# Kernel tuning notes

Hardware: AMD Instinct MI355X
Metric: run time of the kernel (lower is better)

## Reference

```python
import jax, jax.numpy as jnp
import numpy as np

B, N, D, H = 2048, 200, 128, 8

def setup_inputs() -> dict:
    key = jax.random.key(0)
    k1, k2, k3, k4, k5, k6 = jax.random.split(key, 6)
    return {
        "item_embedding": jax.random.normal(k1, (B, N, D), dtype=jnp.float32),
        "query_embedding": jax.random.normal(k2, (B, D), dtype=jnp.float32),
        "mask": jax.random.randint(k3, (B, N, 1), 0, 2).astype(bool),
        "Wq": jax.random.normal(k4, (D * H, D), dtype=jnp.float32) * 0.05,
        "bq": jax.random.normal(k5, (D * H,), dtype=jnp.float32) * 0.05,
        "Wr": jax.random.normal(k6, (1, H), dtype=jnp.float32) * 0.5,
    }

def reference(item_embedding, query_embedding, mask, Wq, bq, Wr):
    b = query_embedding.shape[0]
    # query projection + tanh, reshape to (B, D, H)
    pq = jnp.tanh(query_embedding @ Wq.T + bq).reshape(b, D, H)
    # batched dot: (B,N,D) @ (B,D,H) -> (B,N,H)
    dotted = jnp.einsum('bnd,bdh->bnh', item_embedding, pq)
    # head reduce: (B,N,H) @ (H,1) -> (B,N,1)
    reduced = dotted @ Wr.T
    scores = reduced - jnp.max(reduced, axis=1, keepdims=True)
    att = jnp.exp(scores) * mask
    denom = jnp.sum(att, axis=1, keepdims=True)
    weight = att / jnp.where(denom < 1e-7, denom + 1.0, denom)
    # weighted sum pooling -> (B, D)
    return jnp.sum(weight * item_embedding, axis=1)
```

## Files before the change

### kernel.cpp

```cpp
#include <hip/hip_runtime.h>

#define BB 2048
#define NN 200
#define DD 128
#define HH 8

__global__ __launch_bounds__(256) void proj_kernel(
    const float* __restrict__ q,
    const float* __restrict__ Wq,
    const float* __restrict__ bq,
    const float* __restrict__ Wr,
    float* __restrict__ v)
{
    __shared__ float wq_s[32][257];
    const int t  = threadIdx.x;
    const int jc = blockIdx.x;
    const int b0 = blockIdx.y * 16;
    const int j  = jc * 256 + t;

    float acc[16];
#pragma unroll
    for (int i = 0; i < 16; ++i) acc[i] = 0.f;

    for (int kt = 0; kt < 4; ++kt) {
        __syncthreads();
#pragma unroll
        for (int i = 0; i < 8; ++i) {
            int idx = t + 256 * i;
            int jj  = idx >> 3;
            int kf  = idx & 7;
            const float4 w4 = *(const float4*)(Wq + (size_t)(jc*256 + jj)*128 + kt*32 + kf*4);
            wq_s[kf*4+0][jj] = w4.x;
            wq_s[kf*4+1][jj] = w4.y;
            wq_s[kf*4+2][jj] = w4.z;
            wq_s[kf*4+3][jj] = w4.w;
        }
        __syncthreads();

        float wreg[32];
#pragma unroll
        for (int k = 0; k < 32; ++k) wreg[k] = wq_s[k][t];

#pragma unroll
        for (int bb = 0; bb < 16; ++bb) {
            const float* qrow = q + (size_t)(b0 + bb)*128 + kt*32;
            float s = 0.f;
#pragma unroll
            for (int k = 0; k < 32; ++k) s = fmaf(qrow[k], wreg[k], s);
            acc[bb] += s;
        }
    }

    const float bqj = bq[j];
    const float wrh = Wr[j & 7];
    const int   d   = j >> 3;
#pragma unroll
    for (int bb = 0; bb < 16; ++bb) {
        float p = tanhf(acc[bb] + bqj) * wrh;
        p += __shfl_xor(p, 1);
        p += __shfl_xor(p, 2);
        p += __shfl_xor(p, 4);
        if ((t & 7) == 0) v[(size_t)(b0 + bb)*128 + d] = p;
    }
}

__global__ __launch_bounds__(512) void attn_kernel(
    const float* __restrict__ item,
    const int*   __restrict__ mask,
    const float* __restrict__ v,
    float* __restrict__ out)
{
    __shared__ float item_s[64][132];
    __shared__ float red_s[64];
    __shared__ float w_s[64];
    __shared__ float o_s[4][128];

    const int t   = threadIdx.x;
    const int b   = blockIdx.x;
    const int seg = t & 31;
    const int l64 = t & 63;
    const int d   = t & 127;
    const int p   = t >> 7;

    const float4 vreg  = *(const float4*)(v + (size_t)b*128 + seg*4);
    const float* itemb = item + (size_t)b * (NN * 128);

    float m = -3e38f, lsum = 0.f, o_part = 0.f;

    for (int n0 = 0; n0 < NN; n0 += 64) {
        const int rows = min(64, NN - n0);
        __syncthreads();

#pragma unroll
        for (int i = 0; i < 4; ++i) {
            const int row = (t >> 5) + 16 * i;
            float4 f4 = make_float4(0.f, 0.f, 0.f, 0.f);
            if (row < rows)
                f4 = *(const float4*)(itemb + (size_t)(n0 + row)*128 + seg*4);
            float pp = f4.x*vreg.x + f4.y*vreg.y + f4.z*vreg.z + f4.w*vreg.w;
#pragma unroll
            for (int off = 16; off >= 1; off >>= 1)
                pp += __shfl_xor(pp, off);
            if (row < rows) {
                *(float4*)(&item_s[row][seg*4]) = f4;
                if (seg == 0) red_s[row] = pp;
            }
        }
        __syncthreads();

        float mv = (l64 < rows) ? red_s[l64] : -3e38f;
#pragma unroll
        for (int off = 32; off >= 1; off >>= 1)
            mv = fmaxf(mv, __shfl_xor(mv, off));
        const float new_m = fmaxf(m, mv);
        const float alpha = __expf(m - new_m);
        m = new_m;

        if (t < 64) {
            float w = 0.f;
            if (t < rows) {
                const int mk = mask[(size_t)b * NN + n0 + t];
                w = mk ? __expf(red_s[t] - new_m) : 0.f;
            }
            w_s[t] = w;
        }
        __syncthreads();

        float sv = w_s[l64];
#pragma unroll
        for (int off = 32; off >= 1; off >>= 1)
            sv += __shfl_xor(sv, off);
        lsum = lsum * alpha + sv;

        float acc = 0.f;
#pragma unroll
        for (int nn = 0; nn < 16; ++nn)
            acc = fmaf(w_s[p*16 + nn], item_s[p*16 + nn][d], acc);
        o_part = o_part * alpha + acc;
    }

    o_s[p][d] = o_part;
    __syncthreads();
    if (t < 128) {
        const float tot   = o_s[0][t] + o_s[1][t] + o_s[2][t] + o_s[3][t];
        const float denom = (lsum < 1e-7f) ? (lsum + 1.f) : lsum;
        out[(size_t)b * 128 + t] = tot / denom;
    }
}

extern "C" void kernel_launch(void* const* d_in, const int* in_sizes, int n_in,
                              void* d_out, int out_size, void* d_ws, size_t ws_size,
                              hipStream_t stream) {
    const float* item = (const float*)d_in[0];
    const float* q    = (const float*)d_in[1];
    const int*   mask = (const int*)  d_in[2];
    const float* Wq   = (const float*)d_in[3];
    const float* bq   = (const float*)d_in[4];
    const float* Wr   = (const float*)d_in[5];
    float* out = (float*)d_out;
    float* v   = (float*)d_ws;

    proj_kernel<<<dim3(4, 128), 256, 0, stream>>>(q, Wq, bq, Wr, v);
    attn_kernel<<<dim3(BB), 512, 0, stream>>>(item, mask, v, out);
}
```

Baseline: 345.2 us.

## Register-prefetch next item chunk and restructure attention into three chunks

```diff
diff --git a/kernel.cpp b/kernel.cpp
--- a/kernel.cpp
+++ b/kernel.cpp
@@ -4,6 +4,8 @@
 #define NN 200
 #define DD 128
 #define HH 8
+
+typedef float f4v __attribute__((ext_vector_type(4)));
 
 __global__ __launch_bounds__(256) void proj_kernel(
     const float* __restrict__ q,
@@ -64,51 +66,74 @@
     }
 }
 
-__global__ __launch_bounds__(512) void attn_kernel(
+__global__ __launch_bounds__(512, 8) void attn_kernel(
     const float* __restrict__ item,
     const int*   __restrict__ mask,
     const float* __restrict__ v,
     float* __restrict__ out)
 {
-    __shared__ float item_s[64][132];
-    __shared__ float red_s[64];
-    __shared__ float w_s[64];
-    __shared__ float o_s[4][128];
+    __shared__ float item_s[72][132];
+    __shared__ float red_s[72];
+    __shared__ float w_s[72];
 
-    const int t   = threadIdx.x;
-    const int b   = blockIdx.x;
-    const int seg = t & 31;
-    const int l64 = t & 63;
-    const int d   = t & 127;
-    const int p   = t >> 7;
+    const int t    = threadIdx.x;
+    const int b    = blockIdx.x;
+    const int seg  = t & 31;
+    const int half = t >> 5;
+    const int l64  = t & 63;
+    const int d    = t & 127;
+    const int p    = t >> 7;
 
-    const float4 vreg  = *(const float4*)(v + (size_t)b*128 + seg*4);
+    const f4v vreg = *(const f4v*)(v + (size_t)b*128 + seg*4);
     const float* itemb = item + (size_t)b * (NN * 128);
 
     float m = -3e38f, lsum = 0.f, o_part = 0.f;
 
-    for (int n0 = 0; n0 < NN; n0 += 64) {
-        const int rows = min(64, NN - n0);
+    f4v pre[5];
+#pragma unroll
+    for (int i = 0; i < 5; ++i) {
+        const int row = half + 16*i;
+        pre[i] = (f4v)0.f;
+        if (row < 64)
+            pre[i] = __builtin_nontemporal_load(
+                (const f4v*)(itemb + (size_t)row*128 + seg*4));
+    }
+
+    for (int c = 0; c < 3; ++c) {
+        const int base = c * 64;
+        const int rows = (c == 2) ? 72 : 64;
         __syncthreads();
 
 #pragma unroll
-        for (int i = 0; i < 4; ++i) {
-            const int row = (t >> 5) + 16 * i;
-            float4 f4 = make_float4(0.f, 0.f, 0.f, 0.f);
-            if (row < rows)
-                f4 = *(const float4*)(itemb + (size_t)(n0 + row)*128 + seg*4);
-            float pp = f4.x*vreg.x + f4.y*vreg.y + f4.z*vreg.z + f4.w*vreg.w;
+        for (int i = 0; i < 5; ++i) {
+            const int row = half + 16*i;
+            if (row < rows) {
+                const f4v f = pre[i];
+                float pp = f[0]*vreg[0] + f[1]*vreg[1] + f[2]*vreg[2] + f[3]*vreg[3];
 #pragma unroll
-            for (int off = 16; off >= 1; off >>= 1)
-                pp += __shfl_xor(pp, off);
-            if (row < rows) {
-                *(float4*)(&item_s[row][seg*4]) = f4;
+                for (int off = 16; off >= 1; off >>= 1)
+                    pp += __shfl_xor(pp, off);
+                *(f4v*)(&item_s[row][seg*4]) = f;
                 if (seg == 0) red_s[row] = pp;
+            }
+        }
+
+        if (c < 2) {
+            const int nbase = (c + 1) * 64;
+            const int nrows = (c == 1) ? 72 : 64;
+#pragma unroll
+            for (int i = 0; i < 5; ++i) {
+                const int row = half + 16*i;
+                pre[i] = (f4v)0.f;
+                if (row < nrows)
+                    pre[i] = __builtin_nontemporal_load(
+                        (const f4v*)(itemb + (size_t)(nbase + row)*128 + seg*4));
             }
         }
         __syncthreads();
 
-        float mv = (l64 < rows) ? red_s[l64] : -3e38f;
+        float mv = red_s[l64];
+        if (c == 2 && l64 < 8) mv = fmaxf(mv, red_s[64 + l64]);
 #pragma unroll
         for (int off = 32; off >= 1; off >>= 1)
             mv = fmaxf(mv, __shfl_xor(mv, off));
@@ -116,33 +141,33 @@
         const float alpha = __expf(m - new_m);
         m = new_m;
 
-        if (t < 64) {
-            float w = 0.f;
-            if (t < rows) {
-                const int mk = mask[(size_t)b * NN + n0 + t];
-                w = mk ? __expf(red_s[t] - new_m) : 0.f;
-            }
-            w_s[t] = w;
+        if (t < rows) {
+            const int mk = mask[(size_t)b * NN + base + t];
+            w_s[t] = mk ? __expf(red_s[t] - new_m) : 0.f;
         }
         __syncthreads();
 
         float sv = w_s[l64];
+        if (c == 2 && l64 < 8) sv += w_s[64 + l64];
 #pragma unroll
         for (int off = 32; off >= 1; off >>= 1)
             sv += __shfl_xor(sv, off);
         lsum = lsum * alpha + sv;
 
+        const int rpp = rows >> 2;
         float acc = 0.f;
 #pragma unroll
-        for (int nn = 0; nn < 16; ++nn)
-            acc = fmaf(w_s[p*16 + nn], item_s[p*16 + nn][d], acc);
+        for (int nn = 0; nn < 18; ++nn)
+            if (nn < rpp)
+                acc = fmaf(w_s[p*rpp + nn], item_s[p*rpp + nn][d], acc);
         o_part = o_part * alpha + acc;
     }
 
-    o_s[p][d] = o_part;
+    __syncthreads();
+    item_s[p][d] = o_part;
     __syncthreads();
     if (t < 128) {
-        const float tot   = o_s[0][t] + o_s[1][t] + o_s[2][t] + o_s[3][t];
+        const float tot   = item_s[0][t] + item_s[1][t] + item_s[2][t] + item_s[3][t];
         const float denom = (lsum < 1e-7f) ? (lsum + 1.f) : lsum;
         out[(size_t)b * 128 + t] = tot / denom;
     }
```

After: 343.8 us. Within noise of the previous version (-0.4%).
